# Performance work log

Measured on AMD Instinct MI355X. Metric: run time of the kernel, lower is better.

The kernel has to match this reference:

```python
import jax, jax.numpy as jnp
import numpy as np

CAL_LIST = ["+", "-", "*", "/", "sin", "cos", "exp", "log", "square"]
MAX_MLT = 99999999.0   # overflow cap for * and square
MAX_DIV = 9999.0       # overflow cap for /
MAX_EXP = 17.0         # cap on exp argument
MIN_DENOM = 0.0001     # added to exactly-zero denominators


def _clip_mag(v, mx):
    # Replicates: tmp = abs(mx / v) under no_grad; v * tmp where |v| >= mx
    scale = jax.lax.stop_gradient(jnp.abs(mx / v))
    return jnp.where(jnp.abs(v) >= mx, v * scale, v)


def _apply_ops(x2):
    # x2: [B, variDim]; consumes 2 cols per binary op, 1 per unary op.
    outs = []
    s = 0
    for op in CAL_LIST:
        if op in ("+", "-", "*", "/"):
            a, b = x2[:, s], x2[:, s + 1]
            s += 2
        else:
            a = x2[:, s]
            s += 1
        if op == "+":
            o = a + b
        elif op == "-":
            o = a - b
        elif op == "*":
            o = _clip_mag(a * b, MAX_MLT)
        elif op == "/":
            denom = jnp.where(b == 0.0, b + MIN_DENOM, b)
            o = _clip_mag(a / denom, MAX_DIV)
        elif op == "sin":
            o = jnp.sin(a)
        elif op == "cos":
            o = jnp.cos(a)
        elif op == "exp":
            safe = jnp.where(a >= MAX_EXP, a * jax.lax.stop_gradient(MAX_EXP / a), a)
            o = jnp.exp(safe)
        elif op == "log":
            o = jnp.log(jnp.abs(a))
        elif op == "square":
            o = _clip_mag(a * a, MAX_MLT)
        outs.append(o)
    return jnp.stack(outs, axis=1)  # [B, calNum]


def setup_inputs() -> dict:
    key = jax.random.key(0)
    B = 524288
    vari_num, const_num = 4, 4
    cal_num = len(CAL_LIST)            # 9
    vari_dim = 13                      # sum(opNumList)
    n_layers = 8
    ks = jax.random.split(key, n_layers + 2)
    x = jax.random.normal(ks[0], (B, vari_num + const_num), dtype=jnp.float32)
    inp = {"x": x}
    in_dim = vari_num + const_num
    for i in range(n_layers):
        inp[f"W{i+1}"] = 0.1 * jax.random.normal(ks[i + 1], (vari_dim, in_dim), dtype=jnp.float32)
        in_dim += cal_num              # concat of op outputs with layer input
    inp["Wf"] = 0.1 * jax.random.normal(ks[-1], (1, in_dim), dtype=jnp.float32)
    return inp


def reference(x, W1, W2, W3, W4, W5, W6, W7, W8, Wf):
    h = x
    for W in (W1, W2, W3, W4, W5, W6, W7, W8):
        z = h @ W.T                      # [B, variDim]
        h = jnp.concatenate([_apply_ops(z), h], axis=1)
    return h @ Wf.T                      # [B, 1]
```

## Files before the change

kernel.cpp:

```cpp
#include <hip/hip_runtime.h>
#include <math.h>


static constexpr double MAX_MLT   = 99999999.0;
static constexpr double MAX_DIV   = 9999.0;
static constexpr double MAX_EXP_C = 17.0;
static constexpr double MIN_DENOM = 0.0001;

static constexpr int IN0  = 8;
static constexpr int VDIM = 13;
static constexpr int NOPS = 9;
static constexpr int FDIM = 80;

static constexpr int WSZ[9]  = {104, 221, 338, 455, 572, 689, 806, 923, 80};
static constexpr int WOFF[9] = {0, 104, 325, 663, 1118, 1690, 2379, 3185, 4108};

__global__ void widen_kernel(const float* __restrict__ s0, const float* __restrict__ s1,
                             const float* __restrict__ s2, const float* __restrict__ s3,
                             const float* __restrict__ s4, const float* __restrict__ s5,
                             const float* __restrict__ s6, const float* __restrict__ s7,
                             const float* __restrict__ s8, double* __restrict__ dst) {
    int seg = blockIdx.y;
    int i   = blockIdx.x * blockDim.x + threadIdx.x;
    const float* src;
    switch (seg) {
        case 0: src = s0; break; case 1: src = s1; break; case 2: src = s2; break;
        case 3: src = s3; break; case 4: src = s4; break; case 5: src = s5; break;
        case 6: src = s6; break; case 7: src = s7; break; default: src = s8; break;
    }
    if (i < WSZ[seg]) dst[WOFF[seg] + i] = (double)src[i];
}

struct D2 { double s, c; };
__device__ __attribute__((noinline))
D2 d_sincos2(double as, double ac) {
    D2 r;
    r.s = sin(as);
    r.c = cos(ac);
    return r;
}

__device__ __forceinline__ double clip_ref(double v, double mx) {
    double scale = fabs(mx / v);
    double vs    = v * scale;
    return (fabs(v) >= mx) ? vs : v;
}

template<int IN_DIM, int BASE>
__device__ __forceinline__ void layer_step(const double* __restrict__ W,
                                           double (&h)[FDIM]) {
    double z[VDIM];
    #pragma unroll 2
    for (int j = 0; j < VDIM; ++j) {
        const double* Wr = W + j * IN_DIM;
        double acc = 0.0;
        #pragma unroll
        for (int k = 0; k < IN_DIM; ++k) {
            acc = fma(Wr[k], h[BASE + k], acc);
        }
        z[j] = acc;
    }
    constexpr int BO = BASE - NOPS;
    h[BO + 0] = z[0] + z[1];
    h[BO + 1] = z[2] - z[3];
    h[BO + 2] = clip_ref(z[4] * z[5], MAX_MLT);
    {
        double b     = z[7];
        double denom = (b == 0.0) ? (b + MIN_DENOM) : b;
        h[BO + 3]    = clip_ref(z[6] / denom, MAX_DIV);
    }
    {
        D2 t = d_sincos2(z[8], z[9]);
        h[BO + 4] = t.s;
        h[BO + 5] = t.c;
    }
    {
        double a    = z[10];
        double safe = (a >= MAX_EXP_C) ? (a * (MAX_EXP_C / a)) : a;
        h[BO + 6]   = exp(safe);
    }
    h[BO + 7] = log(fabs(z[11]));
    h[BO + 8] = clip_ref(z[12] * z[12], MAX_MLT);
}

__global__ void __launch_bounds__(64)
net_kernel(const float* __restrict__ x, const double* __restrict__ Wd,
           float* __restrict__ out, int nrows) {
    int row = blockIdx.x * blockDim.x + threadIdx.x;
    if (row >= nrows) return;

    double h[FDIM];

    const float4* x4 = reinterpret_cast<const float4*>(x);
    float4 xa = x4[row * 2 + 0];
    float4 xb = x4[row * 2 + 1];
    h[72] = (double)xa.x; h[73] = (double)xa.y; h[74] = (double)xa.z; h[75] = (double)xa.w;
    h[76] = (double)xb.x; h[77] = (double)xb.y; h[78] = (double)xb.z; h[79] = (double)xb.w;

    layer_step<IN0 + 0 * NOPS, 72>(Wd + WOFF[0], h);
    layer_step<IN0 + 1 * NOPS, 63>(Wd + WOFF[1], h);
    layer_step<IN0 + 2 * NOPS, 54>(Wd + WOFF[2], h);
    layer_step<IN0 + 3 * NOPS, 45>(Wd + WOFF[3], h);
    layer_step<IN0 + 4 * NOPS, 36>(Wd + WOFF[4], h);
    layer_step<IN0 + 5 * NOPS, 27>(Wd + WOFF[5], h);
    layer_step<IN0 + 6 * NOPS, 18>(Wd + WOFF[6], h);
    layer_step<IN0 + 7 * NOPS,  9>(Wd + WOFF[7], h);

    const double* Wf = Wd + WOFF[8];
    double acc = 0.0;
    #pragma unroll
    for (int k = 0; k < FDIM; ++k) {
        acc = fma(Wf[k], h[k], acc);
    }
    out[row] = (float)acc;
}

extern "C" void kernel_launch(void* const* d_in, const int* in_sizes, int n_in,
                              void* d_out, int out_size, void* d_ws, size_t ws_size,
                              hipStream_t stream) {
    const float* x = (const float*)d_in[0];
    double* Wd     = (double*)d_ws;
    float* out     = (float*)d_out;

    {
        dim3 grid((923 + 255) / 256, 9);
        widen_kernel<<<grid, 256, 0, stream>>>(
            (const float*)d_in[1], (const float*)d_in[2], (const float*)d_in[3],
            (const float*)d_in[4], (const float*)d_in[5], (const float*)d_in[6],
            (const float*)d_in[7], (const float*)d_in[8], (const float*)d_in[9],
            Wd);
    }

    int nrows = in_sizes[0] / IN0;
    int block = 64;
    int grid  = (nrows + block - 1) / block;
    net_kernel<<<grid, block, 0, stream>>>(x, Wd, out, nrows);
}
```

Baseline: 276.0 us.

## Stage weights in shared memory and fuse widening into main kernel

Removes the separate float-to-double weight conversion kernel and instead has each block convert and stage all weights into LDS before computing rows. Block size rises from 64 to 256 so the staging cost is spread over more rows. This saves a kernel launch, but replaces uniform scalar global loads with LDS reads, adds per-block conversion work, and uses about 33 KB of shared memory per block, which may limit occupancy.

After: 315.0 us. +14.2%, slower.

```diff
diff --git a/kernel.cpp b/kernel.cpp
--- a/kernel.cpp
+++ b/kernel.cpp
@@ -14,22 +14,7 @@
 
 static constexpr int WSZ[9]  = {104, 221, 338, 455, 572, 689, 806, 923, 80};
 static constexpr int WOFF[9] = {0, 104, 325, 663, 1118, 1690, 2379, 3185, 4108};
-
-__global__ void widen_kernel(const float* __restrict__ s0, const float* __restrict__ s1,
-                             const float* __restrict__ s2, const float* __restrict__ s3,
-                             const float* __restrict__ s4, const float* __restrict__ s5,
-                             const float* __restrict__ s6, const float* __restrict__ s7,
-                             const float* __restrict__ s8, double* __restrict__ dst) {
-    int seg = blockIdx.y;
-    int i   = blockIdx.x * blockDim.x + threadIdx.x;
-    const float* src;
-    switch (seg) {
-        case 0: src = s0; break; case 1: src = s1; break; case 2: src = s2; break;
-        case 3: src = s3; break; case 4: src = s4; break; case 5: src = s5; break;
-        case 6: src = s6; break; case 7: src = s7; break; default: src = s8; break;
-    }
-    if (i < WSZ[seg]) dst[WOFF[seg] + i] = (double)src[i];
-}
+static constexpr int WTOT    = 4188;
 
 struct D2 { double s, c; };
 __device__ __attribute__((noinline))
@@ -83,9 +68,29 @@
     h[BO + 8] = clip_ref(z[12] * z[12], MAX_MLT);
 }
 
-__global__ void __launch_bounds__(64)
-net_kernel(const float* __restrict__ x, const double* __restrict__ Wd,
+__global__ void __launch_bounds__(256)
+net_kernel(const float* __restrict__ x,
+           const float* __restrict__ W1, const float* __restrict__ W2,
+           const float* __restrict__ W3, const float* __restrict__ W4,
+           const float* __restrict__ W5, const float* __restrict__ W6,
+           const float* __restrict__ W7, const float* __restrict__ W8,
+           const float* __restrict__ WfIn,
            float* __restrict__ out, int nrows) {
+    __shared__ double Wl[WTOT];
+
+    {
+        const float* srcs[9] = {W1, W2, W3, W4, W5, W6, W7, W8, WfIn};
+        #pragma unroll
+        for (int s = 0; s < 9; ++s) {
+            const float* src = srcs[s];
+            double*      dst = Wl + WOFF[s];
+            for (int i = threadIdx.x; i < WSZ[s]; i += 256) {
+                dst[i] = (double)src[i];
+            }
+        }
+        __syncthreads();
+    }
+
     int row = blockIdx.x * blockDim.x + threadIdx.x;
     if (row >= nrows) return;
 
@@ -97,16 +102,16 @@
     h[72] = (double)xa.x; h[73] = (double)xa.y; h[74] = (double)xa.z; h[75] = (double)xa.w;
     h[76] = (double)xb.x; h[77] = (double)xb.y; h[78] = (double)xb.z; h[79] = (double)xb.w;
 
-    layer_step<IN0 + 0 * NOPS, 72>(Wd + WOFF[0], h);
-    layer_step<IN0 + 1 * NOPS, 63>(Wd + WOFF[1], h);
-    layer_step<IN0 + 2 * NOPS, 54>(Wd + WOFF[2], h);
-    layer_step<IN0 + 3 * NOPS, 45>(Wd + WOFF[3], h);
-    layer_step<IN0 + 4 * NOPS, 36>(Wd + WOFF[4], h);
-    layer_step<IN0 + 5 * NOPS, 27>(Wd + WOFF[5], h);
-    layer_step<IN0 + 6 * NOPS, 18>(Wd + WOFF[6], h);
-    layer_step<IN0 + 7 * NOPS,  9>(Wd + WOFF[7], h);
+    layer_step<IN0 + 0 * NOPS, 72>(Wl + WOFF[0], h);
+    layer_step<IN0 + 1 * NOPS, 63>(Wl + WOFF[1], h);
+    layer_step<IN0 + 2 * NOPS, 54>(Wl + WOFF[2], h);
+    layer_step<IN0 + 3 * NOPS, 45>(Wl + WOFF[3], h);
+    layer_step<IN0 + 4 * NOPS, 36>(Wl + WOFF[4], h);
+    layer_step<IN0 + 5 * NOPS, 27>(Wl + WOFF[5], h);
+    layer_step<IN0 + 6 * NOPS, 18>(Wl + WOFF[6], h);
+    layer_step<IN0 + 7 * NOPS,  9>(Wl + WOFF[7], h);
 
-    const double* Wf = Wd + WOFF[8];
+    const double* Wf = Wl + WOFF[8];
     double acc = 0.0;
     #pragma unroll
     for (int k = 0; k < FDIM; ++k) {
@@ -119,20 +124,15 @@
                               void* d_out, int out_size, void* d_ws, size_t ws_size,
                               hipStream_t stream) {
     const float* x = (const float*)d_in[0];
-    double* Wd     = (double*)d_ws;
     float* out     = (float*)d_out;
 
-    {
-        dim3 grid((923 + 255) / 256, 9);
-        widen_kernel<<<grid, 256, 0, stream>>>(
-            (const float*)d_in[1], (const float*)d_in[2], (const float*)d_in[3],
-            (const float*)d_in[4], (const float*)d_in[5], (const float*)d_in[6],
-            (const float*)d_in[7], (const float*)d_in[8], (const float*)d_in[9],
-            Wd);
-    }
-
     int nrows = in_sizes[0] / IN0;
-    int block = 64;
+    int block = 256;
     int grid  = (nrows + block - 1) / block;
-    net_kernel<<<grid, block, 0, stream>>>(x, Wd, out, nrows);
+    net_kernel<<<grid, block, 0, stream>>>(
+        x,
+        (const float*)d_in[1], (const float*)d_in[2], (const float*)d_in[3],
+        (const float*)d_in[4], (const float*)d_in[5], (const float*)d_in[6],
+        (const float*)d_in[7], (const float*)d_in[8], (const float*)d_in[9],
+        out, nrows);
 }
```
